# Kernel tuning notes

Hardware: AMD Instinct MI355X
Metric: run time of the kernel (lower is better)

Reference implementation:

```python
import jax, jax.numpy as jnp
import numpy as np
from jax.ops import segment_sum

N_NODES = 50000
N_EDGES = 800000
HIDDEN = 96
N_CLASSES = 10
N_GRAPHS = 64


def gcn_conv(x, W, b, src, dst, num_nodes):
    """PyG GCNConv: symmetric-normalized aggregation with self-loops.
    out = D^{-1/2} (A + I) D^{-1/2} (x W) + b, with D the degree of A + I.
    Self-loop contribution handled analytically instead of appending edges.
    """
    ones = jnp.ones((src.shape[0],), dtype=x.dtype)
    deg = segment_sum(ones, dst, num_segments=num_nodes) + 1.0  # +1 for self-loop
    dinv = jax.lax.rsqrt(deg)
    h = x @ W  # [N, H] small GEMM
    norm = dinv[src] * dinv[dst]  # [E]
    msg = h[src] * norm[:, None]  # [E, H] dominant gather
    out = segment_sum(msg, dst, num_segments=num_nodes)  # scatter-add
    out = out + h * (dinv * dinv)[:, None]  # self-loop term
    return out + b


def setup_inputs() -> dict:
    key = jax.random.key(0)
    ks = jax.random.split(key, 12)
    x = jax.random.normal(ks[0], (N_NODES, HIDDEN), dtype=jnp.float32)
    edge_index = jax.random.randint(ks[1], (2, N_EDGES), 0, N_NODES, dtype=jnp.int64)
    batch = jnp.sort(jax.random.randint(ks[2], (N_NODES,), 0, N_GRAPHS, dtype=jnp.int64))
    s = 1.0 / np.sqrt(HIDDEN)
    W0 = jax.random.normal(ks[3], (HIDDEN, HIDDEN), dtype=jnp.float32) * s
    b0 = jnp.zeros((HIDDEN,), dtype=jnp.float32)
    W1 = jax.random.normal(ks[4], (HIDDEN, HIDDEN), dtype=jnp.float32) * s
    b1 = jnp.zeros((HIDDEN,), dtype=jnp.float32)
    W2 = jax.random.normal(ks[5], (HIDDEN, HIDDEN), dtype=jnp.float32) * s
    b2 = jnp.zeros((HIDDEN,), dtype=jnp.float32)
    W_lin = jax.random.normal(ks[6], (HIDDEN, N_CLASSES), dtype=jnp.float32) * s
    b_lin = jnp.zeros((N_CLASSES,), dtype=jnp.float32)
    return {"x": x, "edge_index": edge_index, "batch": batch,
            "W0": W0, "b0": b0, "W1": W1, "b1": b1, "W2": W2, "b2": b2,
            "W_lin": W_lin, "b_lin": b_lin}


def reference(x, edge_index, batch, W0, b0, W1, b1, W2, b2, W_lin, b_lin):
    src, dst = edge_index[0], edge_index[1]
    n = x.shape[0]
    h = jax.nn.relu(gcn_conv(x, W0, b0, src, dst, n))
    h = jax.nn.relu(gcn_conv(h, W1, b1, src, dst, n))
    h = gcn_conv(h, W2, b2, src, dst, n)  # last layer: no activation
    # global_mean_pool over batch index
    sums = segment_sum(h, batch, num_segments=N_GRAPHS)  # [G, H]
    cnts = segment_sum(jnp.ones((n,), dtype=h.dtype), batch, num_segments=N_GRAPHS)
    pooled = sums / jnp.maximum(cnts, 1.0)[:, None]
    # dropout is identity in eval mode
    return pooled @ W_lin + b_lin  # [G, num_classes]
```

## Files before the change

### kernel.cpp

```cpp
#include <hip/hip_runtime.h>
#include <hip/hip_bf16.h>

#define HID 96
#define NGRAPHS 64

typedef __attribute__((ext_vector_type(8))) short short8;
typedef __attribute__((ext_vector_type(4))) float floatx4;

__device__ __forceinline__ float bf16_to_f32(unsigned short u) {
    unsigned int v = ((unsigned int)u) << 16;
    return __builtin_bit_cast(float, v);
}
__device__ __forceinline__ unsigned short f32_to_bf16(float f) {
    unsigned int u = __builtin_bit_cast(unsigned int, f);
    u += 0x7fff + ((u >> 16) & 1);
    return (unsigned short)(u >> 16);
}

__global__ void deg_kernel(const int* __restrict__ dst, int* __restrict__ deg,
                           int n_edges) {
    int t = blockIdx.x * blockDim.x + threadIdx.x;
    int e0 = t * 4;
    if (e0 + 4 <= n_edges) {
        int4 d4 = *(const int4*)(dst + e0);
        atomicAdd(&deg[d4.x], 1);
        atomicAdd(&deg[d4.y], 1);
        atomicAdd(&deg[d4.z], 1);
        atomicAdd(&deg[d4.w], 1);
    } else {
        for (int e = e0; e < n_edges; e++) atomicAdd(&deg[dst[e]], 1);
    }
}

__global__ void dinv_kernel(const int* __restrict__ deg, float* __restrict__ dinv,
                            int n) {
    int i = blockIdx.x * blockDim.x + threadIdx.x;
    if (i < n) dinv[i] = rsqrtf((float)deg[i] + 1.0f);
}

__global__ __launch_bounds__(256) void scan_phaseA(const int* __restrict__ deg,
                                                   int* __restrict__ blocksum,
                                                   int N) {
    int i = blockIdx.x * 256 + threadIdx.x;
    int v = (i < N) ? deg[i] : 0;
#pragma unroll
    for (int off = 32; off > 0; off >>= 1) v += __shfl_down(v, off, 64);
    __shared__ int s[4];
    if ((threadIdx.x & 63) == 0) s[threadIdx.x >> 6] = v;
    __syncthreads();
    if (threadIdx.x == 0) blocksum[blockIdx.x] = s[0] + s[1] + s[2] + s[3];
}

__global__ __launch_bounds__(256) void scan_phaseB(int* __restrict__ blocksum,
                                                   int* __restrict__ blockoff,
                                                   int nblocks, int* __restrict__ rowptr,
                                                   int N, int E) {
    __shared__ int s[256];
    int t = threadIdx.x;
    int own = (t < nblocks) ? blocksum[t] : 0;
    s[t] = own;
    __syncthreads();
#pragma unroll
    for (int off = 1; off < 256; off <<= 1) {
        int v = (t >= off) ? s[t - off] : 0;
        __syncthreads();
        s[t] += v;
        __syncthreads();
    }
    if (t < nblocks) blockoff[t] = s[t] - own;
    if (t == 0) rowptr[N] = E;
}

__global__ __launch_bounds__(256) void scan_phaseC(const int* __restrict__ deg,
                                                   const int* __restrict__ blockoff,
                                                   int* __restrict__ rowptr,
                                                   int* __restrict__ cursor, int N) {
    __shared__ int s[256];
    int t = threadIdx.x;
    int i = blockIdx.x * 256 + t;
    int own = (i < N) ? deg[i] : 0;
    s[t] = own;
    __syncthreads();
#pragma unroll
    for (int off = 1; off < 256; off <<= 1) {
        int v = (t >= off) ? s[t - off] : 0;
        __syncthreads();
        s[t] += v;
        __syncthreads();
    }
    if (i < N) {
        int r = blockoff[blockIdx.x] + s[t] - own;
        rowptr[i] = r;
        cursor[i] = r;
    }
}

__global__ void csr_fill(const int* __restrict__ src, const int* __restrict__ dst,
                         int* __restrict__ cursor,
                         unsigned short* __restrict__ csr_src, int n_edges) {
    int t = blockIdx.x * blockDim.x + threadIdx.x;
    int e0 = t * 4;
    if (e0 + 4 <= n_edges) {
        int4 d4 = *(const int4*)(dst + e0);
        int4 s4 = *(const int4*)(src + e0);
        int p0 = atomicAdd(&cursor[d4.x], 1);
        int p1 = atomicAdd(&cursor[d4.y], 1);
        int p2 = atomicAdd(&cursor[d4.z], 1);
        int p3 = atomicAdd(&cursor[d4.w], 1);
        csr_src[p0] = (unsigned short)s4.x;
        csr_src[p1] = (unsigned short)s4.y;
        csr_src[p2] = (unsigned short)s4.z;
        csr_src[p3] = (unsigned short)s4.w;
    } else {
        for (int e = e0; e < n_edges; e++) {
            int p = atomicAdd(&cursor[dst[e]], 1);
            csr_src[p] = (unsigned short)src[e];
        }
    }
}

__global__ void cvt_f32_bf16(const float* __restrict__ in,
                             unsigned short* __restrict__ out, int n4) {
    int i = blockIdx.x * blockDim.x + threadIdx.x;
    if (i < n4) {
        float4 v = *(const float4*)(in + i * 4);
        ushort4 o;
        o.x = f32_to_bf16(v.x);
        o.y = f32_to_bf16(v.y);
        o.z = f32_to_bf16(v.z);
        o.w = f32_to_bf16(v.w);
        *(ushort4*)(out + i * 4) = o;
    }
}

__global__ void swizzle_W(const float* __restrict__ W0, const float* __restrict__ W1,
                          const float* __restrict__ W2, unsigned short* __restrict__ Wz) {
    const float* W = (blockIdx.x == 0) ? W0 : (blockIdx.x == 1) ? W1 : W2;
    unsigned short* dst = Wz + blockIdx.x * HID * HID;
    for (int e = threadIdx.x; e < HID * HID; e += blockDim.x) {
        int k = e / HID, n = e % HID;
        int nt = n >> 4, kki = k >> 5, quad = (k >> 3) & 3, j = k & 7;
        int lane = (n & 15) | (quad << 4);
        dst[(((nt * 3 + kki) * 64 + lane) << 3) | j] = f32_to_bf16(W[e]);
    }
}

__global__ __launch_bounds__(256) void gemm_mfma(
    const unsigned short* __restrict__ A, const unsigned short* __restrict__ Wz,
    const float* __restrict__ dinv, unsigned short* __restrict__ Out, int Mtiles) {
    int wave = threadIdx.x >> 6;
    int lane = threadIdx.x & 63;
    int quad = lane >> 4;
    int mrow = lane & 15;

    short8 bfrag[18];
    const short8* Wz8 = (const short8*)Wz;
#pragma unroll
    for (int f = 0; f < 18; f++) bfrag[f] = Wz8[f * 64 + lane];

    for (int tt = blockIdx.x * 4 + wave; tt < Mtiles; tt += gridDim.x * 4) {
        int m0 = tt * 16;
        const unsigned short* arow = A + (size_t)(m0 + mrow) * HID + quad * 8;
        short8 a0 = *(const short8*)(arow);
        short8 a1 = *(const short8*)(arow + 32);
        short8 a2 = *(const short8*)(arow + 64);
        float dscale[4];
#pragma unroll
        for (int r = 0; r < 4; r++) dscale[r] = dinv[m0 + quad * 4 + r];
        floatx4 acc[6];
#pragma unroll
        for (int nt = 0; nt < 6; nt++) {
            floatx4 c = {0.0f, 0.0f, 0.0f, 0.0f};
            c = __builtin_amdgcn_mfma_f32_16x16x32_bf16(a0, bfrag[nt * 3 + 0], c, 0, 0, 0);
            c = __builtin_amdgcn_mfma_f32_16x16x32_bf16(a1, bfrag[nt * 3 + 1], c, 0, 0, 0);
            c = __builtin_amdgcn_mfma_f32_16x16x32_bf16(a2, bfrag[nt * 3 + 2], c, 0, 0, 0);
            acc[nt] = c;
        }
        unsigned short* orow = Out + (size_t)m0 * HID;
#pragma unroll
        for (int nt = 0; nt < 6; nt++)
#pragma unroll
            for (int r = 0; r < 4; r++) {
                int row = quad * 4 + r;
                orow[(size_t)row * HID + nt * 16 + mrow] =
                    f32_to_bf16(acc[nt][r] * dscale[r]);
            }
    }
}

__global__ __launch_bounds__(256) void gcn_gather_bf16(
    const unsigned short* __restrict__ h, const int* __restrict__ rowptr,
    const unsigned short* __restrict__ csr_src, const float* __restrict__ dinv,
    const float* __restrict__ b, unsigned short* __restrict__ out, int N,
    int do_relu) {
    int wv = threadIdx.x >> 6;
    int lane = threadIdx.x & 63;
    int n = blockIdx.x * 4 + wv;
    if (n >= N) return;
    int fi = (lane < 48) ? lane * 2 : 94;
    int start = rowptr[n];
    int end = rowptr[n + 1];
    float di = dinv[n];

    ushort2 hv = *(const ushort2*)(h + (size_t)n * HID + fi);
    float acc0 = bf16_to_f32(hv.x);
    float acc1 = bf16_to_f32(hv.y);

    int i = start;
    for (; i + 8 <= end; i += 8) {
        int s0 = csr_src[i + 0];
        int s1 = csr_src[i + 1];
        int s2 = csr_src[i + 2];
        int s3 = csr_src[i + 3];
        int s4 = csr_src[i + 4];
        int s5 = csr_src[i + 5];
        int s6 = csr_src[i + 6];
        int s7 = csr_src[i + 7];
        ushort2 v0 = *(const ushort2*)(h + (size_t)s0 * HID + fi);
        ushort2 v1 = *(const ushort2*)(h + (size_t)s1 * HID + fi);
        ushort2 v2 = *(const ushort2*)(h + (size_t)s2 * HID + fi);
        ushort2 v3 = *(const ushort2*)(h + (size_t)s3 * HID + fi);
        ushort2 v4 = *(const ushort2*)(h + (size_t)s4 * HID + fi);
        ushort2 v5 = *(const ushort2*)(h + (size_t)s5 * HID + fi);
        ushort2 v6 = *(const ushort2*)(h + (size_t)s6 * HID + fi);
        ushort2 v7 = *(const ushort2*)(h + (size_t)s7 * HID + fi);
        acc0 += bf16_to_f32(v0.x) + bf16_to_f32(v1.x) + bf16_to_f32(v2.x) +
                bf16_to_f32(v3.x) + bf16_to_f32(v4.x) + bf16_to_f32(v5.x) +
                bf16_to_f32(v6.x) + bf16_to_f32(v7.x);
        acc1 += bf16_to_f32(v0.y) + bf16_to_f32(v1.y) + bf16_to_f32(v2.y) +
                bf16_to_f32(v3.y) + bf16_to_f32(v4.y) + bf16_to_f32(v5.y) +
                bf16_to_f32(v6.y) + bf16_to_f32(v7.y);
    }
#pragma unroll 4
    for (; i < end; i++) {
        int s = csr_src[i];
        ushort2 v = *(const ushort2*)(h + (size_t)s * HID + fi);
        acc0 += bf16_to_f32(v.x);
        acc1 += bf16_to_f32(v.y);
    }
    acc0 = acc0 * di + b[fi];
    acc1 = acc1 * di + b[fi + 1];
    if (do_relu) {
        acc0 = fmaxf(acc0, 0.0f);
        acc1 = fmaxf(acc1, 0.0f);
    }
    if (lane < 48) {
        ushort2 o;
        o.x = f32_to_bf16(acc0);
        o.y = f32_to_bf16(acc1);
        *(ushort2*)(out + (size_t)n * HID + fi) = o;
    }
}

#define PCH 32
__global__ __launch_bounds__(96) void pool_kernel(
    const unsigned short* __restrict__ h, const int* __restrict__ batch,
    float* __restrict__ sums, float* __restrict__ cnts, int N) {
    int n0 = blockIdx.x * PCH;
    if (n0 >= N) return;
    int f = threadIdx.x;
    int nend = min(n0 + PCH, N);
    int gfirst = batch[n0];
    int glast = batch[nend - 1];
    if (gfirst == glast) {
        float acc = 0.0f;
#pragma unroll 8
        for (int n = n0; n < nend; n++) acc += bf16_to_f32(h[(size_t)n * HID + f]);
        atomicAdd(&sums[gfirst * HID + f], acc);
        if (f == 0) atomicAdd(&cnts[gfirst], (float)(nend - n0));
        return;
    }
    int g_cur = gfirst;
    float acc = 0.0f, cacc = 0.0f;
    for (int n = n0; n < nend; n++) {
        int g = batch[n];
        if (g != g_cur) {
            atomicAdd(&sums[g_cur * HID + f], acc);
            if (f == 0) atomicAdd(&cnts[g_cur], cacc);
            acc = 0.0f;
            cacc = 0.0f;
            g_cur = g;
        }
        acc += bf16_to_f32(h[(size_t)n * HID + f]);
        cacc += 1.0f;
    }
    atomicAdd(&sums[g_cur * HID + f], acc);
    if (f == 0) atomicAdd(&cnts[g_cur], cacc);
}

__global__ __launch_bounds__(640) void final_kernel(
    const float* __restrict__ sums, const float* __restrict__ cnts,
    const float* __restrict__ Wlin, const float* __restrict__ blin,
    float* __restrict__ out) {
    int t = threadIdx.x;
    if (t >= NGRAPHS * 10) return;
    int g = t / 10;
    int c = t % 10;
    float denom = fmaxf(cnts[g], 1.0f);
    float acc = blin[c];
#pragma unroll
    for (int f = 0; f < HID; f++)
        acc += (sums[g * HID + f] / denom) * Wlin[f * 10 + c];
    out[t] = acc;
}

extern "C" void kernel_launch(void* const* d_in, const int* in_sizes, int n_in,
                              void* d_out, int out_size, void* d_ws,
                              size_t ws_size, hipStream_t stream) {
    const float* x = (const float*)d_in[0];
    const int* edge = (const int*)d_in[1];
    const int* batch = (const int*)d_in[2];
    const float* W[3] = {(const float*)d_in[3], (const float*)d_in[5],
                         (const float*)d_in[7]};
    const float* B[3] = {(const float*)d_in[4], (const float*)d_in[6],
                         (const float*)d_in[8]};
    const float* Wlin = (const float*)d_in[9];
    const float* blin = (const float*)d_in[10];
    float* out = (float*)d_out;

    int N = in_sizes[0] / HID;
    int E = in_sizes[1] / 2;
    const int* src = edge;
    const int* dst = edge + E;
    int NB = (N + 255) / 256;

    char* ws = (char*)d_ws;
    size_t off = 0;
    auto alloc = [&](size_t bytes) {
        void* p = ws + off;
        off += (bytes + 255) & ~(size_t)255;
        return p;
    };
    int* deg = (int*)alloc((size_t)N * 4);
    float* dinv = (float*)alloc((size_t)N * 4);
    int* rowptr = (int*)alloc(((size_t)N + 1) * 4);
    int* cursor = (int*)alloc((size_t)N * 4);
    int* blocksum = (int*)alloc((size_t)NB * 4);
    int* blockoff = (int*)alloc((size_t)NB * 4);
    unsigned short* csr_src = (unsigned short*)alloc((size_t)E * 2);
    unsigned short* Wz = (unsigned short*)alloc(3 * HID * HID * 2);
    unsigned short* bufx = (unsigned short*)alloc((size_t)N * HID * 2);
    unsigned short* bufh = (unsigned short*)alloc((size_t)N * HID * 2);
    unsigned short* bufa = (unsigned short*)alloc((size_t)N * HID * 2);
    float* psum = (float*)alloc(NGRAPHS * HID * 4);
    float* pcnt = (float*)alloc(NGRAPHS * 4);

    hipMemsetAsync(deg, 0, (size_t)N * 4, stream);
    deg_kernel<<<(E / 4 + 255) / 256, 256, 0, stream>>>(dst, deg, E);
    dinv_kernel<<<(N + 255) / 256, 256, 0, stream>>>(deg, dinv, N);
    scan_phaseA<<<NB, 256, 0, stream>>>(deg, blocksum, N);
    scan_phaseB<<<1, 256, 0, stream>>>(blocksum, blockoff, NB, rowptr, N, E);
    scan_phaseC<<<NB, 256, 0, stream>>>(deg, blockoff, rowptr, cursor, N);
    csr_fill<<<(E / 4 + 255) / 256, 256, 0, stream>>>(src, dst, cursor, csr_src, E);
    swizzle_W<<<3, 256, 0, stream>>>(W[0], W[1], W[2], Wz);
    cvt_f32_bf16<<<((size_t)N * HID / 4 + 255) / 256, 256, 0, stream>>>(
        x, bufx, N * HID / 4);

    int Mtiles = (N + 15) / 16;
    int gather_grid = (N + 3) / 4;

    unsigned short* act_in = bufx;
    unsigned short* act_out = bufa;
    for (int l = 0; l < 3; l++) {
        gemm_mfma<<<640, 256, 0, stream>>>(act_in, Wz + l * HID * HID, dinv,
                                           bufh, Mtiles);
        gcn_gather_bf16<<<gather_grid, 256, 0, stream>>>(
            bufh, rowptr, csr_src, dinv, B[l], act_out, N, l < 2);
        unsigned short* t = act_in;
        act_in = act_out;
        act_out = t;
    }
    hipMemsetAsync(psum, 0, (NGRAPHS * HID + NGRAPHS) * sizeof(float), stream);
    pool_kernel<<<(N + PCH - 1) / PCH, 96, 0, stream>>>(act_in, batch, psum,
                                                        pcnt, N);
    final_kernel<<<1, 640, 0, stream>>>(psum, pcnt, Wlin, blin, out);
}
```

Before: 338.6 us.

## Fuse gather with next-layer GEMM and pooling, pad CSR rows to multiples of 8

Each neighbour list in the CSR is padded to a multiple of 8 with a sentinel index that points at a zeroed row, so the gather loop can fetch eight indices per vector load and needs no remainder loop. Each layer's gather is fused with the following layer's MFMA GEMM through an LDS tile, the final gather is fused with mean pooling, and the first GEMM reads fp32 input directly, which drops the separate conversion, pool and dinv kernels. This removes intermediate activation round trips and several launches. The cost is that 16 nodes are processed serially per wave, which reduces parallelism, and the CSR buffer grows because of the padding.

```diff
diff --git a/kernel.cpp b/kernel.cpp
--- a/kernel.cpp
+++ b/kernel.cpp
@@ -3,9 +3,12 @@
 
 #define HID 96
 #define NGRAPHS 64
+#define SENT 0xC3C3u
+#define NROWS 50116
 
 typedef __attribute__((ext_vector_type(8))) short short8;
 typedef __attribute__((ext_vector_type(4))) float floatx4;
+typedef __attribute__((ext_vector_type(8))) unsigned short ushort8v;
 
 __device__ __forceinline__ float bf16_to_f32(unsigned short u) {
     unsigned int v = ((unsigned int)u) << 16;
@@ -32,17 +35,14 @@
     }
 }
 
-__global__ void dinv_kernel(const int* __restrict__ deg, float* __restrict__ dinv,
-                            int n) {
-    int i = blockIdx.x * blockDim.x + threadIdx.x;
-    if (i < n) dinv[i] = rsqrtf((float)deg[i] + 1.0f);
-}
-
 __global__ __launch_bounds__(256) void scan_phaseA(const int* __restrict__ deg,
+                                                   float* __restrict__ dinv,
                                                    int* __restrict__ blocksum,
                                                    int N) {
     int i = blockIdx.x * 256 + threadIdx.x;
-    int v = (i < N) ? deg[i] : 0;
+    int d = (i < N) ? deg[i] : 0;
+    if (i < N) dinv[i] = rsqrtf((float)d + 1.0f);
+    int v = (d + 7) & ~7;
 #pragma unroll
     for (int off = 32; off > 0; off >>= 1) v += __shfl_down(v, off, 64);
     __shared__ int s[4];
@@ -53,8 +53,7 @@
 
 __global__ __launch_bounds__(256) void scan_phaseB(int* __restrict__ blocksum,
                                                    int* __restrict__ blockoff,
-                                                   int nblocks, int* __restrict__ rowptr,
-                                                   int N, int E) {
+                                                   int nblocks) {
     __shared__ int s[256];
     int t = threadIdx.x;
     int own = (t < nblocks) ? blocksum[t] : 0;
@@ -68,7 +67,6 @@
         __syncthreads();
     }
     if (t < nblocks) blockoff[t] = s[t] - own;
-    if (t == 0) rowptr[N] = E;
 }
 
 __global__ __launch_bounds__(256) void scan_phaseC(const int* __restrict__ deg,
@@ -78,7 +76,7 @@
     __shared__ int s[256];
     int t = threadIdx.x;
     int i = blockIdx.x * 256 + t;
-    int own = (i < N) ? deg[i] : 0;
+    int own = (i < N) ? (deg[i] + 7) & ~7 : 0;
     s[t] = own;
     __syncthreads();
 #pragma unroll
@@ -92,6 +90,7 @@
         int r = blockoff[blockIdx.x] + s[t] - own;
         rowptr[i] = r;
         cursor[i] = r;
+        if (i == N - 1) rowptr[N] = r + own;
     }
 }
 
@@ -119,20 +118,6 @@
     }
 }
 
-__global__ void cvt_f32_bf16(const float* __restrict__ in,
-                             unsigned short* __restrict__ out, int n4) {
-    int i = blockIdx.x * blockDim.x + threadIdx.x;
-    if (i < n4) {
-        float4 v = *(const float4*)(in + i * 4);
-        ushort4 o;
-        o.x = f32_to_bf16(v.x);
-        o.y = f32_to_bf16(v.y);
-        o.z = f32_to_bf16(v.z);
-        o.w = f32_to_bf16(v.w);
-        *(ushort4*)(out + i * 4) = o;
-    }
-}
-
 __global__ void swizzle_W(const float* __restrict__ W0, const float* __restrict__ W1,
                           const float* __restrict__ W2, unsigned short* __restrict__ Wz) {
     const float* W = (blockIdx.x == 0) ? W0 : (blockIdx.x == 1) ? W1 : W2;
@@ -145,147 +130,196 @@
     }
 }
 
-__global__ __launch_bounds__(256) void gemm_mfma(
-    const unsigned short* __restrict__ A, const unsigned short* __restrict__ Wz,
+__global__ void zero_sentinel(unsigned short* __restrict__ a,
+                              unsigned short* __restrict__ b) {
+    int t = threadIdx.x;
+    a[(size_t)SENT * HID + t] = 0;
+    b[(size_t)SENT * HID + t] = 0;
+}
+
+__global__ __launch_bounds__(256) void gemm0_f32(
+    const float* __restrict__ X, const unsigned short* __restrict__ Wz,
     const float* __restrict__ dinv, unsigned short* __restrict__ Out, int Mtiles) {
     int wave = threadIdx.x >> 6;
     int lane = threadIdx.x & 63;
     int quad = lane >> 4;
     int mrow = lane & 15;
+    int tt = blockIdx.x * 4 + wave;
+    if (tt >= Mtiles) return;
 
     short8 bfrag[18];
     const short8* Wz8 = (const short8*)Wz;
 #pragma unroll
     for (int f = 0; f < 18; f++) bfrag[f] = Wz8[f * 64 + lane];
 
-    for (int tt = blockIdx.x * 4 + wave; tt < Mtiles; tt += gridDim.x * 4) {
-        int m0 = tt * 16;
-        const unsigned short* arow = A + (size_t)(m0 + mrow) * HID + quad * 8;
-        short8 a0 = *(const short8*)(arow);
-        short8 a1 = *(const short8*)(arow + 32);
-        short8 a2 = *(const short8*)(arow + 64);
-        float dscale[4];
-#pragma unroll
-        for (int r = 0; r < 4; r++) dscale[r] = dinv[m0 + quad * 4 + r];
-        floatx4 acc[6];
-#pragma unroll
-        for (int nt = 0; nt < 6; nt++) {
-            floatx4 c = {0.0f, 0.0f, 0.0f, 0.0f};
-            c = __builtin_amdgcn_mfma_f32_16x16x32_bf16(a0, bfrag[nt * 3 + 0], c, 0, 0, 0);
-            c = __builtin_amdgcn_mfma_f32_16x16x32_bf16(a1, bfrag[nt * 3 + 1], c, 0, 0, 0);
-            c = __builtin_amdgcn_mfma_f32_16x16x32_bf16(a2, bfrag[nt * 3 + 2], c, 0, 0, 0);
-            acc[nt] = c;
-        }
-        unsigned short* orow = Out + (size_t)m0 * HID;
-#pragma unroll
-        for (int nt = 0; nt < 6; nt++)
-#pragma unroll
-            for (int r = 0; r < 4; r++) {
-                int row = quad * 4 + r;
-                orow[(size_t)row * HID + nt * 16 + mrow] =
-                    f32_to_bf16(acc[nt][r] * dscale[r]);
-            }
-    }
-}
-
-__global__ __launch_bounds__(256) void gcn_gather_bf16(
+    int m0 = tt * 16;
+    const float* arow = X + (size_t)(m0 + mrow) * HID + quad * 8;
+    short8 a[3];
+#pragma unroll
+    for (int kb = 0; kb < 3; kb++) {
+        float4 u = *(const float4*)(arow + kb * 32);
+        float4 v = *(const float4*)(arow + kb * 32 + 4);
+        short8 t;
+        t[0] = (short)f32_to_bf16(u.x); t[1] = (short)f32_to_bf16(u.y);
+        t[2] = (short)f32_to_bf16(u.z); t[3] = (short)f32_to_bf16(u.w);
+        t[4] = (short)f32_to_bf16(v.x); t[5] = (short)f32_to_bf16(v.y);
+        t[6] = (short)f32_to_bf16(v.z); t[7] = (short)f32_to_bf16(v.w);
+        a[kb] = t;
+    }
+    float dscale[4];
+#pragma unroll
+    for (int r = 0; r < 4; r++) dscale[r] = dinv[m0 + quad * 4 + r];
+    unsigned short* orow = Out + (size_t)m0 * HID;
+#pragma unroll
+    for (int nt = 0; nt < 6; nt++) {
+        floatx4 c = {0.0f, 0.0f, 0.0f, 0.0f};
+        c = __builtin_amdgcn_mfma_f32_16x16x32_bf16(a[0], bfrag[nt * 3 + 0], c, 0, 0, 0);
+        c = __builtin_amdgcn_mfma_f32_16x16x32_bf16(a[1], bfrag[nt * 3 + 1], c, 0, 0, 0);
+        c = __builtin_amdgcn_mfma_f32_16x16x32_bf16(a[2], bfrag[nt * 3 + 2], c, 0, 0, 0);
+#pragma unroll
+        for (int r = 0; r < 4; r++)
+            orow[(size_t)(quad * 4 + r) * HID + nt * 16 + mrow] =
+                f32_to_bf16(c[r] * dscale[r]);
+    }
+}
+
+__global__ __launch_bounds__(256) void fused_gather_gemm(
     const unsigned short* __restrict__ h, const int* __restrict__ rowptr,
-    const unsigned short* __restrict__ csr_src, const float* __restrict__ dinv,
-    const float* __restrict__ b, unsigned short* __restrict__ out, int N,
-    int do_relu) {
+    const unsigned short* __restrict__ csr, const float* __restrict__ dinv,
+    const float* __restrict__ bias, const unsigned short* __restrict__ Wz,
+    unsigned short* __restrict__ Out, int Mtiles) {
+    __shared__ unsigned short tile[4][16][104];
     int wv = threadIdx.x >> 6;
     int lane = threadIdx.x & 63;
-    int n = blockIdx.x * 4 + wv;
-    if (n >= N) return;
+    int quad = lane >> 4;
+    int mrow = lane & 15;
+    int tt = blockIdx.x * 4 + wv;
+    if (tt >= Mtiles) return;
     int fi = (lane < 48) ? lane * 2 : 94;
-    int start = rowptr[n];
-    int end = rowptr[n + 1];
-    float di = dinv[n];
-
-    ushort2 hv = *(const ushort2*)(h + (size_t)n * HID + fi);
-    float acc0 = bf16_to_f32(hv.x);
-    float acc1 = bf16_to_f32(hv.y);
-
-    int i = start;
-    for (; i + 8 <= end; i += 8) {
-        int s0 = csr_src[i + 0];
-        int s1 = csr_src[i + 1];
-        int s2 = csr_src[i + 2];
-        int s3 = csr_src[i + 3];
-        int s4 = csr_src[i + 4];
-        int s5 = csr_src[i + 5];
-        int s6 = csr_src[i + 6];
-        int s7 = csr_src[i + 7];
-        ushort2 v0 = *(const ushort2*)(h + (size_t)s0 * HID + fi);
-        ushort2 v1 = *(const ushort2*)(h + (size_t)s1 * HID + fi);
-        ushort2 v2 = *(const ushort2*)(h + (size_t)s2 * HID + fi);
-        ushort2 v3 = *(const ushort2*)(h + (size_t)s3 * HID + fi);
-        ushort2 v4 = *(const ushort2*)(h + (size_t)s4 * HID + fi);
-        ushort2 v5 = *(const ushort2*)(h + (size_t)s5 * HID + fi);
-        ushort2 v6 = *(const ushort2*)(h + (size_t)s6 * HID + fi);
-        ushort2 v7 = *(const ushort2*)(h + (size_t)s7 * HID + fi);
-        acc0 += bf16_to_f32(v0.x) + bf16_to_f32(v1.x) + bf16_to_f32(v2.x) +
-                bf16_to_f32(v3.x) + bf16_to_f32(v4.x) + bf16_to_f32(v5.x) +
-                bf16_to_f32(v6.x) + bf16_to_f32(v7.x);
-        acc1 += bf16_to_f32(v0.y) + bf16_to_f32(v1.y) + bf16_to_f32(v2.y) +
-                bf16_to_f32(v3.y) + bf16_to_f32(v4.y) + bf16_to_f32(v5.y) +
-                bf16_to_f32(v6.y) + bf16_to_f32(v7.y);
-    }
-#pragma unroll 4
-    for (; i < end; i++) {
-        int s = csr_src[i];
-        ushort2 v = *(const ushort2*)(h + (size_t)s * HID + fi);
-        acc0 += bf16_to_f32(v.x);
-        acc1 += bf16_to_f32(v.y);
-    }
-    acc0 = acc0 * di + b[fi];
-    acc1 = acc1 * di + b[fi + 1];
-    if (do_relu) {
-        acc0 = fmaxf(acc0, 0.0f);
-        acc1 = fmaxf(acc1, 0.0f);
-    }
-    if (lane < 48) {
-        ushort2 o;
-        o.x = f32_to_bf16(acc0);
-        o.y = f32_to_bf16(acc1);
-        *(ushort2*)(out + (size_t)n * HID + fi) = o;
-    }
-}
-
-#define PCH 32
-__global__ __launch_bounds__(96) void pool_kernel(
-    const unsigned short* __restrict__ h, const int* __restrict__ batch,
-    float* __restrict__ sums, float* __restrict__ cnts, int N) {
-    int n0 = blockIdx.x * PCH;
-    if (n0 >= N) return;
-    int f = threadIdx.x;
-    int nend = min(n0 + PCH, N);
-    int gfirst = batch[n0];
-    int glast = batch[nend - 1];
-    if (gfirst == glast) {
-        float acc = 0.0f;
-#pragma unroll 8
-        for (int n = n0; n < nend; n++) acc += bf16_to_f32(h[(size_t)n * HID + f]);
-        atomicAdd(&sums[gfirst * HID + f], acc);
-        if (f == 0) atomicAdd(&cnts[gfirst], (float)(nend - n0));
-        return;
-    }
-    int g_cur = gfirst;
-    float acc = 0.0f, cacc = 0.0f;
-    for (int n = n0; n < nend; n++) {
+    float b0 = bias[fi], b1 = bias[fi + 1];
+
+    short8 bfrag[18];
+    const short8* Wz8 = (const short8*)Wz;
+#pragma unroll
+    for (int f = 0; f < 18; f++) bfrag[f] = Wz8[f * 64 + lane];
+
+    int n0 = tt * 16;
+    for (int j = 0; j < 16; j++) {
+        int n = n0 + j;
+        int i = rowptr[n];
+        int end = rowptr[n + 1];
+        float di = dinv[n];
+        ushort2 hv = *(const ushort2*)(h + (size_t)n * HID + fi);
+        float a0 = bf16_to_f32(hv.x);
+        float a1 = bf16_to_f32(hv.y);
+        for (; i < end; i += 8) {
+            ushort8v iv = *(const ushort8v*)(csr + i);
+            ushort2 v0 = *(const ushort2*)(h + (size_t)iv[0] * HID + fi);
+            ushort2 v1 = *(const ushort2*)(h + (size_t)iv[1] * HID + fi);
+            ushort2 v2 = *(const ushort2*)(h + (size_t)iv[2] * HID + fi);
+            ushort2 v3 = *(const ushort2*)(h + (size_t)iv[3] * HID + fi);
+            ushort2 v4 = *(const ushort2*)(h + (size_t)iv[4] * HID + fi);
+            ushort2 v5 = *(const ushort2*)(h + (size_t)iv[5] * HID + fi);
+            ushort2 v6 = *(const ushort2*)(h + (size_t)iv[6] * HID + fi);
+            ushort2 v7 = *(const ushort2*)(h + (size_t)iv[7] * HID + fi);
+            a0 += bf16_to_f32(v0.x) + bf16_to_f32(v1.x) + bf16_to_f32(v2.x) +
+                  bf16_to_f32(v3.x) + bf16_to_f32(v4.x) + bf16_to_f32(v5.x) +
+                  bf16_to_f32(v6.x) + bf16_to_f32(v7.x);
+            a1 += bf16_to_f32(v0.y) + bf16_to_f32(v1.y) + bf16_to_f32(v2.y) +
+                  bf16_to_f32(v3.y) + bf16_to_f32(v4.y) + bf16_to_f32(v5.y) +
+                  bf16_to_f32(v6.y) + bf16_to_f32(v7.y);
+        }
+        a0 = fmaxf(a0 * di + b0, 0.0f);
+        a1 = fmaxf(a1 * di + b1, 0.0f);
+        if (lane < 48) {
+            tile[wv][j][fi] = f32_to_bf16(a0);
+            tile[wv][j][fi + 1] = f32_to_bf16(a1);
+        }
+    }
+    const unsigned short* tp = &tile[wv][0][0];
+    short8 a[3];
+#pragma unroll
+    for (int kb = 0; kb < 3; kb++)
+        a[kb] = *(const short8*)(tp + mrow * 104 + quad * 8 + kb * 32);
+    float dscale[4];
+#pragma unroll
+    for (int r = 0; r < 4; r++) dscale[r] = dinv[n0 + quad * 4 + r];
+    unsigned short* orow = Out + (size_t)n0 * HID;
+#pragma unroll
+    for (int nt = 0; nt < 6; nt++) {
+        floatx4 c = {0.0f, 0.0f, 0.0f, 0.0f};
+        c = __builtin_amdgcn_mfma_f32_16x16x32_bf16(a[0], bfrag[nt * 3 + 0], c, 0, 0, 0);
+        c = __builtin_amdgcn_mfma_f32_16x16x32_bf16(a[1], bfrag[nt * 3 + 1], c, 0, 0, 0);
+        c = __builtin_amdgcn_mfma_f32_16x16x32_bf16(a[2], bfrag[nt * 3 + 2], c, 0, 0, 0);
+#pragma unroll
+        for (int r = 0; r < 4; r++)
+            orow[(size_t)(quad * 4 + r) * HID + nt * 16 + mrow] =
+                f32_to_bf16(c[r] * dscale[r]);
+    }
+}
+
+__global__ __launch_bounds__(256) void gather_pool(
+    const unsigned short* __restrict__ h, const int* __restrict__ rowptr,
+    const unsigned short* __restrict__ csr, const float* __restrict__ dinv,
+    const float* __restrict__ bias, const int* __restrict__ batch,
+    float* __restrict__ psum, float* __restrict__ pcnt, int Mtiles) {
+    int wv = threadIdx.x >> 6;
+    int lane = threadIdx.x & 63;
+    int tt = blockIdx.x * 4 + wv;
+    if (tt >= Mtiles) return;
+    int fi = (lane < 48) ? lane * 2 : 94;
+    float b0 = bias[fi], b1 = bias[fi + 1];
+
+    int n0 = tt * 16;
+    int g_cur = batch[n0];
+    float s0 = 0.0f, s1 = 0.0f;
+    int cnt = 0;
+    for (int j = 0; j < 16; j++) {
+        int n = n0 + j;
+        int i = rowptr[n];
+        int end = rowptr[n + 1];
+        float di = dinv[n];
+        ushort2 hv = *(const ushort2*)(h + (size_t)n * HID + fi);
+        float a0 = bf16_to_f32(hv.x);
+        float a1 = bf16_to_f32(hv.y);
+        for (; i < end; i += 8) {
+            ushort8v iv = *(const ushort8v*)(csr + i);
+            ushort2 v0 = *(const ushort2*)(h + (size_t)iv[0] * HID + fi);
+            ushort2 v1 = *(const ushort2*)(h + (size_t)iv[1] * HID + fi);
+            ushort2 v2 = *(const ushort2*)(h + (size_t)iv[2] * HID + fi);
+            ushort2 v3 = *(const ushort2*)(h + (size_t)iv[3] * HID + fi);
+            ushort2 v4 = *(const ushort2*)(h + (size_t)iv[4] * HID + fi);
+            ushort2 v5 = *(const ushort2*)(h + (size_t)iv[5] * HID + fi);
+            ushort2 v6 = *(const ushort2*)(h + (size_t)iv[6] * HID + fi);
+            ushort2 v7 = *(const ushort2*)(h + (size_t)iv[7] * HID + fi);
+            a0 += bf16_to_f32(v0.x) + bf16_to_f32(v1.x) + bf16_to_f32(v2.x) +
+                  bf16_to_f32(v3.x) + bf16_to_f32(v4.x) + bf16_to_f32(v5.x) +
+                  bf16_to_f32(v6.x) + bf16_to_f32(v7.x);
+            a1 += bf16_to_f32(v0.y) + bf16_to_f32(v1.y) + bf16_to_f32(v2.y) +
+                  bf16_to_f32(v3.y) + bf16_to_f32(v4.y) + bf16_to_f32(v5.y) +
+                  bf16_to_f32(v6.y) + bf16_to_f32(v7.y);
+        }
+        a0 = a0 * di + b0;
+        a1 = a1 * di + b1;
         int g = batch[n];
         if (g != g_cur) {
-            atomicAdd(&sums[g_cur * HID + f], acc);
-            if (f == 0) atomicAdd(&cnts[g_cur], cacc);
-            acc = 0.0f;
-            cacc = 0.0f;
+            if (lane < 48) {
+                atomicAdd(&psum[g_cur * HID + fi], s0);
+                atomicAdd(&psum[g_cur * HID + fi + 1], s1);
+            }
+            if (lane == 0) atomicAdd(&pcnt[g_cur], (float)cnt);
+            s0 = 0.0f; s1 = 0.0f; cnt = 0;
             g_cur = g;
         }
-        acc += bf16_to_f32(h[(size_t)n * HID + f]);
-        cacc += 1.0f;
-    }
-    atomicAdd(&sums[g_cur * HID + f], acc);
-    if (f == 0) atomicAdd(&cnts[g_cur], cacc);
+        s0 += a0;
+        s1 += a1;
+        cnt++;
+    }
+    if (lane < 48) {
+        atomicAdd(&psum[g_cur * HID + fi], s0);
+        atomicAdd(&psum[g_cur * HID + fi + 1], s1);
+    }
+    if (lane == 0) atomicAdd(&pcnt[g_cur], (float)cnt);
 }
 
 __global__ __launch_bounds__(640) void final_kernel(
@@ -337,41 +371,34 @@
     int* cursor = (int*)alloc((size_t)N * 4);
     int* blocksum = (int*)alloc((size_t)NB * 4);
     int* blockoff = (int*)alloc((size_t)NB * 4);
-    unsigned short* csr_src = (unsigned short*)alloc((size_t)E * 2);
+    size_t csr_cap = (size_t)E + 8 * (size_t)N;
+    unsigned short* csr_src = (unsigned short*)alloc(csr_cap * 2);
     unsigned short* Wz = (unsigned short*)alloc(3 * HID * HID * 2);
-    unsigned short* bufx = (unsigned short*)alloc((size_t)N * HID * 2);
-    unsigned short* bufh = (unsigned short*)alloc((size_t)N * HID * 2);
-    unsigned short* bufa = (unsigned short*)alloc((size_t)N * HID * 2);
-    float* psum = (float*)alloc(NGRAPHS * HID * 4);
-    float* pcnt = (float*)alloc(NGRAPHS * 4);
+    unsigned short* bufA = (unsigned short*)alloc((size_t)NROWS * HID * 2);
+    unsigned short* bufB = (unsigned short*)alloc((size_t)NROWS * HID * 2);
+    float* psum = (float*)alloc((NGRAPHS * HID + NGRAPHS) * 4);
+    float* pcnt = psum + NGRAPHS * HID;
 
     hipMemsetAsync(deg, 0, (size_t)N * 4, stream);
+    hipMemsetAsync(csr_src, 0xC3, csr_cap * 2, stream);
+    hipMemsetAsync(psum, 0, (NGRAPHS * HID + NGRAPHS) * 4, stream);
     deg_kernel<<<(E / 4 + 255) / 256, 256, 0, stream>>>(dst, deg, E);
-    dinv_kernel<<<(N + 255) / 256, 256, 0, stream>>>(deg, dinv, N);
-    scan_phaseA<<<NB, 256, 0, stream>>>(deg, blocksum, N);
-    scan_phaseB<<<1, 256, 0, stream>>>(blocksum, blockoff, NB, rowptr, N, E);
+    scan_phaseA<<<NB, 256, 0, stream>>>(deg, dinv, blocksum, N);
+    scan_phaseB<<<1, 256, 0, stream>>>(blocksum, blockoff, NB);
     scan_phaseC<<<NB, 256, 0, stream>>>(deg, blockoff, rowptr, cursor, N);
     csr_fill<<<(E / 4 + 255) / 256, 256, 0, stream>>>(src, dst, cursor, csr_src, E);
     swizzle_W<<<3, 256, 0, stream>>>(W[0], W[1], W[2], Wz);
-    cvt_f32_bf16<<<((size_t)N * HID / 4 + 255) / 256, 256, 0, stream>>>(
-        x, bufx, N * HID / 4);
+    zero_sentinel<<<1, HID, 0, stream>>>(bufA, bufB);
 
     int Mtiles = (N + 15) / 16;
-    int gather_grid = (N + 3) / 4;
-
-    unsigned short* act_in = bufx;
-    unsigned short* act_out = bufa;
-    for (int l = 0; l < 3; l++) {
-        gemm_mfma<<<640, 256, 0, stream>>>(act_in, Wz + l * HID * HID, dinv,
-                                           bufh, Mtiles);
-        gcn_gather_bf16<<<gather_grid, 256, 0, stream>>>(
-            bufh, rowptr, csr_src, dinv, B[l], act_out, N, l < 2);
-        unsigned short* t = act_in;
-        act_in = act_out;
-        act_out = t;
-    }
-    hipMemsetAsync(psum, 0, (NGRAPHS * HID + NGRAPHS) * sizeof(float), stream);
-    pool_kernel<<<(N + PCH - 1) / PCH, 96, 0, stream>>>(act_in, batch, psum,
-                                                        pcnt, N);
+    int grid16 = (Mtiles + 3) / 4;
+
+    gemm0_f32<<<grid16, 256, 0, stream>>>(x, Wz, dinv, bufA, Mtiles);
+    fused_gather_gemm<<<grid16, 256, 0, stream>>>(
+        bufA, rowptr, csr_src, dinv, B[0], Wz + 1 * HID * HID, bufB, Mtiles);
+    fused_gather_gemm<<<grid16, 256, 0, stream>>>(
+        bufB, rowptr, csr_src, dinv, B[1], Wz + 2 * HID * HID, bufA, Mtiles);
+    gather_pool<<<grid16, 256, 0, stream>>>(bufA, rowptr, csr_src, dinv, B[2],
+                                            batch, psum, pcnt, Mtiles);
     final_kernel<<<1, 640, 0, stream>>>(psum, pcnt, Wlin, blin, out);
 }
```

Result: no change. 342.2 us (+1.1%).
